# Kernel tuning notes

Measured on AMD Instinct MI355X. Metric: run time of the kernel, lower is better.

Reference implementation:

```python
import jax, jax.numpy as jnp
import numpy as np

DIM = 512
BATCH, SEQ = 4, 4096


def setup_inputs() -> dict:
    key = jax.random.key(0)
    kx, kq, kk, kv, ko = jax.random.split(key, 5)
    s = DIM ** -0.5  # fan-in style init scale for stability
    return {
        "x": jax.random.normal(kx, (BATCH, SEQ, DIM), dtype=jnp.float32),
        "Wq": jax.random.normal(kq, (DIM, DIM), dtype=jnp.float32) * s,
        "Wk": jax.random.normal(kk, (DIM, DIM), dtype=jnp.float32) * s,
        "Wv": jax.random.normal(kv, (DIM, DIM), dtype=jnp.float32) * s,
        "Wo": jax.random.normal(ko, (DIM, DIM), dtype=jnp.float32) * s,
    }


def reference(x, Wq, Wk, Wv, Wo):
    # x: [B, S, D]; projections (torch Linear, no bias -> x @ W here)
    q = jnp.einsum('bsd,dk->bsk', x, Wq)  # [B,S,K]
    k = jnp.einsum('bsd,dk->bsk', x, Wk)  # [B,S,K]
    v = jnp.einsum('bsd,dv->bsv', x, Wv)  # [B,S,V]

    # sequential recurrence: M_t = M_{t-1} + v_t k_t^T ; y_t = M_t q_t
    def step(M, qkv_t):
        q_t, k_t, v_t = qkv_t  # each [B, K] / [B, V]
        M = M + v_t[:, :, None] * k_t[:, None, :]  # [B, V, K]
        y_t = jnp.einsum('bvk,bk->bv', M, q_t)
        return M, y_t

    M0 = jnp.zeros((x.shape[0], Wv.shape[1], Wk.shape[1]), dtype=x.dtype)
    qT = jnp.swapaxes(q, 0, 1)  # [S,B,K]
    kT = jnp.swapaxes(k, 0, 1)
    vT = jnp.swapaxes(v, 0, 1)
    _, ys = jax.lax.scan(step, M0, (qT, kT, vT))  # ys: [S,B,V]
    y = jnp.swapaxes(ys, 0, 1)  # [B,S,V]
    return jnp.einsum('bsv,vd->bsd', y, Wo)
```

## Files before the change

### kernel.cpp

```cpp
#include <hip/hip_runtime.h>
#include <hip/hip_bf16.h>

typedef __attribute__((ext_vector_type(8))) short bf16x8;
typedef __attribute__((ext_vector_type(4))) float f32x4;

__device__ inline short f2bf(float f) {
    __hip_bfloat16 h = __float2bfloat16(f);
    short s;
    __builtin_memcpy(&s, &h, 2);
    return s;
}
__device__ inline float bf2f(short s) {
    unsigned int u = ((unsigned int)(unsigned short)s) << 16;
    float f;
    __builtin_memcpy(&f, &u, 4);
    return f;
}

__device__ inline void cp16_async(const void* g, void* l) {
    __builtin_amdgcn_global_load_lds(
        (const __attribute__((address_space(1))) void*)g,
        (__attribute__((address_space(3))) void*)l, 16, 0, 0);
}

__global__ void prep_kernel(const float* __restrict__ x, short* __restrict__ Xp,
                            const float* __restrict__ W0, const float* __restrict__ W1,
                            const float* __restrict__ W2, const float* __restrict__ W3,
                            short* __restrict__ PW, short* __restrict__ WoT) {
    int bid = blockIdx.x;
    if (bid < 4096) {
        int f = bid * 256 + threadIdx.x;
        int mtf = f >> 13, r = f & 8191, kb = r >> 7, row = r & 127;
        const float* src = x + ((size_t)(mtf * 128 + row) * 512 + kb * 8);
        float4 a = ((const float4*)src)[0];
        float4 bq = ((const float4*)src)[1];
        short t[8];
        t[0] = f2bf(a.x);  t[1] = f2bf(a.y);  t[2] = f2bf(a.z);  t[3] = f2bf(a.w);
        t[4] = f2bf(bq.x); t[5] = f2bf(bq.y); t[6] = f2bf(bq.z); t[7] = f2bf(bq.w);
        ((int4*)Xp)[f] = *(const int4*)t;
    } else if (bid < 4480) {
        int g = (bid - 4096) * 256 + threadIdx.x;
        int lane = g & 63, ksg = (g >> 6) & 15, nn = g >> 10;
        int w = nn >> 5;
        int nl = (nn & 31) * 16 + (lane & 15);
        int k0 = ksg * 32 + (lane >> 4) * 8;
        const float* W = (w == 0) ? W0 : (w == 1) ? W1 : W2;
        short t[8];
#pragma unroll
        for (int e = 0; e < 8; ++e) t[e] = f2bf(W[(size_t)(k0 + e) * 512 + nl]);
        ((int4*)PW)[g] = *(const int4*)t;
    } else {
        int i = (bid - 4480) * 256 + threadIdx.x;
        int n = i >> 9, k = i & 511;
        WoT[i] = f2bf(W3[k * 512 + n]);
    }
}


#define KSTEP(ks) { \
    bf16x8 af[4], bfr[4]; \
    _Pragma("unroll") for (int i = 0; i < 4; ++i) \
        af[i] = *(const bf16x8*)&Xs[((ks) * 512 + quad * 128 + wm * 64 + i * 16 + lr) * 8]; \
    _Pragma("unroll") for (int j = 0; j < 4; ++j) \
        bfr[j] = *(const bf16x8*)&PB[((size_t)((j * 16 + (ks)) * 64 + lane)) * 8]; \
    _Pragma("unroll") for (int i = 0; i < 4; ++i) \
        _Pragma("unroll") for (int j = 0; j < 4; ++j) \
            acc[i * 4 + j] = __builtin_amdgcn_mfma_f32_16x16x32_bf16(af[i], bfr[j], acc[i * 4 + j], 0, 0, 0); }

__global__ __launch_bounds__(512, 2) void proj_qkv(const short* __restrict__ Xp,
                                                   const short* __restrict__ PW,
                                                   short* __restrict__ Qb, short* __restrict__ Kb,
                                                   short* __restrict__ Vt, short* __restrict__ Kt) {
    __shared__ short Xs[65536];
    const int tid = threadIdx.x, lane = tid & 63, wv = tid >> 6;
    const int lr = lane & 15, quad = lane >> 4;
    const int wm = wv >> 2, wn = wv & 3;
    const int bid = blockIdx.x;
    const int swz = (bid & 7) * 32 + (bid >> 3);
    const int mt = swz >> 1, half = swz & 1;
    const short* Ap = Xp + (size_t)mt * 65536;
#pragma unroll
    for (int j = 0; j < 8; ++j) {
        const int f = j * 512 + tid;
        cp16_async(Ap + (size_t)f * 8, (char*)Xs + f * 16);
    }
    __builtin_amdgcn_sched_barrier(0);
#pragma unroll
    for (int j = 8; j < 16; ++j) {
        const int f = j * 512 + tid;
        cp16_async(Ap + (size_t)f * 8, (char*)Xs + f * 16);
    }
    __builtin_amdgcn_sched_barrier(0);
    const int b = mt >> 5;
    const int tl0 = (mt & 31) * 128 + wm * 64;
    const int trow0 = mt * 128 + wm * 64;
    for (int pass = 0; pass < 3; ++pass) {
        const int gc0 = half * 768 + pass * 256;
        f32x4 acc[16];
#pragma unroll
        for (int i = 0; i < 16; ++i) acc[i] = (f32x4){0.f, 0.f, 0.f, 0.f};
        const short* PB = PW + (size_t)((gc0 >> 4) + wn * 4) * 8192;
        if (pass == 0) {
            asm volatile("s_waitcnt vmcnt(8)" ::: "memory");
            __builtin_amdgcn_sched_barrier(0);
            __builtin_amdgcn_s_barrier();
            __builtin_amdgcn_sched_barrier(0);
#pragma unroll 4
            for (int ks = 0; ks < 8; ++ks) KSTEP(ks)
            __builtin_amdgcn_sched_barrier(0);
            asm volatile("s_waitcnt vmcnt(0)" ::: "memory");
            __builtin_amdgcn_sched_barrier(0);
            __builtin_amdgcn_s_barrier();
            __builtin_amdgcn_sched_barrier(0);
#pragma unroll 4
            for (int ks = 8; ks < 16; ++ks) KSTEP(ks)
        } else {
#pragma unroll 4
            for (int ks = 0; ks < 16; ++ks) KSTEP(ks)
        }
        const int p = gc0 >> 9;
        const int fc0 = (gc0 & 511) + wn * 64;
        if (p < 2) {
            short* C = p ? Kb : Qb;
#pragma unroll
            for (int i = 0; i < 4; ++i)
#pragma unroll
                for (int j = 0; j < 4; ++j) {
                    const size_t base = (size_t)(trow0 + i * 16 + quad * 4) * 512 + fc0 + j * 16 + lr;
#pragma unroll
                    for (int r = 0; r < 4; ++r)
                        C[base + (size_t)r * 512] = f2bf(acc[i * 4 + j][r]);
                }
        }
        if (p >= 1) {
            short* T = (p == 1) ? Kt : Vt;
#pragma unroll
            for (int i = 0; i < 4; ++i)
#pragma unroll
                for (int j = 0; j < 4; ++j) {
                    const int f = fc0 + j * 16 + lr;
                    short tmp[4];
#pragma unroll
                    for (int r = 0; r < 4; ++r) tmp[r] = f2bf(acc[i * 4 + j][r]);
                    *(int2*)&T[((size_t)b * 512 + f) * 4096 + tl0 + i * 16 + quad * 4] = *(const int2*)tmp;
                }
        }
    }
}


#define LDS_DECL __shared__ short sm[8][4096]

__device__ inline void stage32(const short* __restrict__ A, int lda,
                               const short* __restrict__ B, int ldb, int k0,
                               short* sA, short* sB, int tid) {
#pragma unroll
    for (int j = 0; j < 2; ++j) {
        const int L = tid * 16 + j * 4096;
        const int row = L >> 6;
        const int cb = (L & 63) ^ ((row & 3) << 4);
        cp16_async((const char*)(A + (size_t)row * lda + k0) + cb, (char*)sA + L);
        cp16_async((const char*)(B + (size_t)row * ldb + k0) + cb, (char*)sB + L);
    }
}

__device__ inline void compute32(const short* sA, const short* sB, f32x4* acc,
                                 int wr, int wc, int lr, int quad) {
    const int cb = (quad * 16) ^ ((lr & 3) << 4);
    bf16x8 af[4], bfr[4];
#pragma unroll
    for (int i = 0; i < 4; ++i)
        af[i] = *(const bf16x8*)((const char*)sA + (wr + i * 16 + lr) * 64 + cb);
#pragma unroll
    for (int j = 0; j < 4; ++j)
        bfr[j] = *(const bf16x8*)((const char*)sB + (wc + j * 16 + lr) * 64 + cb);
#pragma unroll
    for (int i = 0; i < 4; ++i)
#pragma unroll
        for (int j = 0; j < 4; ++j)
            acc[i * 4 + j] = __builtin_amdgcn_mfma_f32_16x16x32_bf16(af[i], bfr[j], acc[i * 4 + j], 0, 0, 0);
}

__device__ inline void kloop_pipe(const short* __restrict__ A, int lda,
                                  const short* __restrict__ B, int ldb, int Kd,
                                  f32x4* acc, short (*sm)[4096]) {
    const int tid = threadIdx.x, lane = tid & 63, wv = tid >> 6;
    const int quad = lane >> 4, lr = lane & 15;
    const int wr = (wv >> 1) * 64, wc = (wv & 1) * 64;
    const int NT = Kd >> 5;
    stage32(A, lda, B, ldb, 0,  sm[0], sm[1], tid);
    stage32(A, lda, B, ldb, 32, sm[2], sm[3], tid);
    stage32(A, lda, B, ldb, 64, sm[4], sm[5], tid);
    __builtin_amdgcn_sched_barrier(0);
    asm volatile("s_waitcnt vmcnt(8)" ::: "memory");
    __builtin_amdgcn_sched_barrier(0);
    __builtin_amdgcn_s_barrier();
    __builtin_amdgcn_sched_barrier(0);
    for (int t = 0; t < NT; ++t) {
        const int cur = (t & 3) << 1;
        if (t + 3 < NT)
            stage32(A, lda, B, ldb, (t + 3) << 5,
                    sm[((t + 3) & 3) << 1], sm[(((t + 3) & 3) << 1) + 1], tid);
        __builtin_amdgcn_sched_barrier(0);
        compute32(sm[cur], sm[cur + 1], acc, wr, wc, lr, quad);
        __builtin_amdgcn_sched_barrier(0);
        if (t + 3 < NT) {
            asm volatile("s_waitcnt vmcnt(8)" ::: "memory");
        } else if (t + 2 < NT) {
            asm volatile("s_waitcnt vmcnt(4)" ::: "memory");
        } else {
            asm volatile("s_waitcnt vmcnt(0)" ::: "memory");
        }
        __builtin_amdgcn_sched_barrier(0);
        __builtin_amdgcn_s_barrier();
        __builtin_amdgcn_sched_barrier(0);
    }
}

__device__ inline void store_out(float* p, float v) { *p = v; }
__device__ inline void store_out(short* p, float v) { *p = f2bf(v); }

template <typename OutT>
__device__ inline void store_tile128(OutT* C, int ldc, const f32x4* acc) {
    const int lane = threadIdx.x & 63, wv = threadIdx.x >> 6;
    const int quad = lane >> 4, lr = lane & 15;
    const int wr = (wv >> 1) * 64, wc = (wv & 1) * 64;
#pragma unroll
    for (int i = 0; i < 4; ++i)
#pragma unroll
        for (int j = 0; j < 4; ++j)
#pragma unroll
            for (int r = 0; r < 4; ++r)
                store_out(&C[(size_t)(wr + i * 16 + quad * 4 + r) * ldc + wc + j * 16 + lr],
                          acc[i * 4 + j][r]);
}


__global__ __launch_bounds__(256, 2) void phaseA(const short* __restrict__ Vt,
                                                 const short* __restrict__ Kt,
                                                 short* __restrict__ AM) {
    LDS_DECL;
    const int bc = blockIdx.z, b = bc >> 4, c = bc & 15;
    const short* Ap = Vt + ((size_t)b * 512 + blockIdx.x * 128) * 4096 + c * 256;
    const short* Bp = Kt + ((size_t)b * 512 + blockIdx.y * 128) * 4096 + c * 256;
    short* Cp = AM + (size_t)bc * 262144 + (size_t)blockIdx.x * 128 * 512 + blockIdx.y * 128;
    f32x4 acc[16];
#pragma unroll
    for (int i = 0; i < 16; ++i) acc[i] = (f32x4){0.f, 0.f, 0.f, 0.f};
    kloop_pipe(Ap, 4096, Bp, 4096, 256, acc, sm);
    store_tile128(Cp, 512, acc);
}

__global__ __launch_bounds__(256, 2) void scan_phaseS(short* __restrict__ AM,
                                                      const short* __restrict__ Q,
                                                      const short* __restrict__ K,
                                                      short* __restrict__ P) {
    LDS_DECL;
    if (blockIdx.x < 512) {
        int i = blockIdx.x * 256 + threadIdx.x;
        int b = i >> 15;
        int vk8 = i & 32767;
        size_t base = (size_t)b * 16 * 262144 + (size_t)vk8 * 8;
        float acc[8];
#pragma unroll
        for (int s = 0; s < 8; ++s) acc[s] = 0.f;
        for (int c = 0; c < 16; ++c) {
            short* p = AM + base + (size_t)c * 262144;
            short in8[8];
            *(int4*)in8 = *(const int4*)p;
            short out8[8];
#pragma unroll
            for (int s = 0; s < 8; ++s) out8[s] = f2bf(acc[s]);
            *(int4*)p = *(const int4*)out8;
#pragma unroll
            for (int s = 0; s < 8; ++s) acc[s] += bf2f(in8[s]);
        }
        return;
    }
    const int e = blockIdx.x - 512;
    const int bc = e >> 2, mt = e & 1, nt = (e >> 1) & 1;
    if (mt < nt) return;
    const int b = bc >> 4, c = bc & 15;
    short* Pt = P + (size_t)bc * 65536 + (size_t)mt * 128 * 256 + nt * 128;
    const short* Ap = Q + ((size_t)(b * 4096 + c * 256 + mt * 128)) * 512;
    const short* Bp = K + ((size_t)(b * 4096 + c * 256 + nt * 128)) * 512;
    f32x4 acc[16];
#pragma unroll
    for (int i = 0; i < 16; ++i) acc[i] = (f32x4){0.f, 0.f, 0.f, 0.f};
    kloop_pipe(Ap, 512, Bp, 512, 512, acc, sm);
    const int lane = threadIdx.x & 63, wv = threadIdx.x >> 6;
    const int quad = lane >> 4, lr = lane & 15;
    const int wr = (wv >> 1) * 64, wc = (wv & 1) * 64;
    const bool diag = (mt == nt);
#pragma unroll
    for (int i = 0; i < 4; ++i)
#pragma unroll
        for (int j = 0; j < 4; ++j)
#pragma unroll
            for (int r = 0; r < 4; ++r) {
                int t = wr + i * 16 + quad * 4 + r;
                int jj = wc + j * 16 + lr;
                float v = (!diag || jj <= t) ? acc[i * 4 + j][r] : 0.f;
                Pt[(size_t)t * 256 + jj] = f2bf(v);
            }
}

__global__ __launch_bounds__(256, 2) void phaseY(const short* __restrict__ Q,
                                                 const short* __restrict__ Mpre,
                                                 const short* __restrict__ P,
                                                 const short* __restrict__ Vt,
                                                 short* __restrict__ Y) {
    LDS_DECL;
    const int bc = blockIdx.z, b = bc >> 4, c = bc & 15;
    const int mt = blockIdx.x, nt = blockIdx.y;
    f32x4 acc[16];
#pragma unroll
    for (int i = 0; i < 16; ++i) acc[i] = (f32x4){0.f, 0.f, 0.f, 0.f};
    const short* Ai = Q + ((size_t)(b * 4096 + c * 256 + mt * 128)) * 512;
    const short* Bi = Mpre + (size_t)bc * 262144 + (size_t)nt * 128 * 512;
    kloop_pipe(Ai, 512, Bi, 512, 512, acc, sm);
    const short* Ap = P + (size_t)bc * 65536 + (size_t)mt * 128 * 256;
    const short* Bv = Vt + ((size_t)b * 512 + nt * 128) * 4096 + c * 256;
    kloop_pipe(Ap, 256, Bv, 4096, (mt + 1) * 128, acc, sm);
    short* Cp = Y + ((size_t)(b * 4096 + c * 256 + mt * 128)) * 512 + nt * 128;
    store_tile128(Cp, 512, acc);
}

template <typename OutT>
__global__ __launch_bounds__(256, 2) void gemm128(const short* __restrict__ A, int lda,
                                                  const short* __restrict__ B, int ldb,
                                                  OutT* __restrict__ C, int ldc, int Kd) {
    LDS_DECL;
    const short* At = A + (size_t)blockIdx.x * 128 * lda;
    const short* Bt = B + (size_t)blockIdx.y * 128 * ldb;
    OutT* Ct = C + (size_t)blockIdx.x * 128 * ldc + blockIdx.y * 128;
    f32x4 acc[16];
#pragma unroll
    for (int i = 0; i < 16; ++i) acc[i] = (f32x4){0.f, 0.f, 0.f, 0.f};
    kloop_pipe(At, lda, Bt, ldb, Kd, acc, sm);
    store_tile128(Ct, ldc, acc);
}


extern "C" void kernel_launch(void* const* d_in, const int* in_sizes, int n_in,
                              void* d_out, int out_size, void* d_ws, size_t ws_size,
                              hipStream_t stream) {
    const float* x  = (const float*)d_in[0];
    const float* Wq = (const float*)d_in[1];
    const float* Wk = (const float*)d_in[2];
    const float* Wv = (const float*)d_in[3];
    const float* Wo = (const float*)d_in[4];
    float* out = (float*)d_out;

    const size_t NTD = 16384 * 512;

    short* ws  = (short*)d_ws;
    short* Xp  = ws;
    short* Qb  = Xp + NTD;
    short* Kb  = Qb + NTD;
    short* Kt  = Kb + NTD;
    short* Vt  = Kt + NTD;
    short* P   = Vt + NTD;
    short* W4T = P + 4194304;
    short* AM  = W4T + 1048576;
    short* Yb  = Kb;

    short* PW  = W4T;
    short* WoT = W4T + 786432;

    prep_kernel<<<5504, 256, 0, stream>>>(x, Xp, Wq, Wk, Wv, Wo, PW, WoT);
    proj_qkv<<<256, 512, 0, stream>>>(Xp, PW, Qb, Kb, Vt, Kt);
    phaseA<<<dim3(4, 4, 64), 256, 0, stream>>>(Vt, Kt, AM);
    scan_phaseS<<<768, 256, 0, stream>>>(AM, Qb, Kb, P);
    phaseY<<<dim3(2, 4, 64), 256, 0, stream>>>(Qb, AM, P, Vt, Yb);
    gemm128<float><<<dim3(128, 4), 256, 0, stream>>>(Yb, 512, WoT, 512, out, 512, 512);
}
```

Baseline: 223.7 us.

## Replace pipelined 128x128 GEMMs with LDS-resident A-panel kernels streaming B from global

Rewrites phaseA, scan_phaseS, phaseY and the output GEMM to use 512-thread blocks. Each block stages one full A panel into swizzled LDS once, and each wave reads its B fragments straight from global memory instead of running a 4-stage double-tile LDS pipeline. Larger per-block tiles reduce the number of blocks and the amount of redundant A traffic. The output GEMM is transposed so each lane writes a float4 vector. The cost is B loads that skip LDS and are not coalesced across waves, fewer blocks to fill the GPU, and more accumulators per thread in phaseA.

```diff
diff --git a/kernel.cpp b/kernel.cpp
--- a/kernel.cpp
+++ b/kernel.cpp
@@ -22,6 +22,7 @@
         (const __attribute__((address_space(1))) void*)g,
         (__attribute__((address_space(3))) void*)l, 16, 0, 0);
 }
+
 
 __global__ void prep_kernel(const float* __restrict__ x, short* __restrict__ Xp,
                             const float* __restrict__ W0, const float* __restrict__ W1,
@@ -71,7 +72,7 @@
                                                    const short* __restrict__ PW,
                                                    short* __restrict__ Qb, short* __restrict__ Kb,
                                                    short* __restrict__ Vt, short* __restrict__ Kt) {
-    __shared__ short Xs[65536];
+    __shared__ __attribute__((aligned(16))) short Xs[65536];
     const int tid = threadIdx.x, lane = tid & 63, wv = tid >> 6;
     const int lr = lane & 15, quad = lane >> 4;
     const int wm = wv >> 2, wn = wv & 3;
@@ -149,115 +150,83 @@
 }
 
 
-#define LDS_DECL __shared__ short sm[8][4096]
-
-__device__ inline void stage32(const short* __restrict__ A, int lda,
-                               const short* __restrict__ B, int ldb, int k0,
-                               short* sA, short* sB, int tid) {
-#pragma unroll
-    for (int j = 0; j < 2; ++j) {
-        const int L = tid * 16 + j * 4096;
-        const int row = L >> 6;
-        const int cb = (L & 63) ^ ((row & 3) << 4);
-        cp16_async((const char*)(A + (size_t)row * lda + k0) + cb, (char*)sA + L);
-        cp16_async((const char*)(B + (size_t)row * ldb + k0) + cb, (char*)sB + L);
-    }
-}
-
-__device__ inline void compute32(const short* sA, const short* sB, f32x4* acc,
-                                 int wr, int wc, int lr, int quad) {
-    const int cb = (quad * 16) ^ ((lr & 3) << 4);
-    bf16x8 af[4], bfr[4];
-#pragma unroll
-    for (int i = 0; i < 4; ++i)
-        af[i] = *(const bf16x8*)((const char*)sA + (wr + i * 16 + lr) * 64 + cb);
-#pragma unroll
-    for (int j = 0; j < 4; ++j)
-        bfr[j] = *(const bf16x8*)((const char*)sB + (wc + j * 16 + lr) * 64 + cb);
-#pragma unroll
-    for (int i = 0; i < 4; ++i)
-#pragma unroll
-        for (int j = 0; j < 4; ++j)
-            acc[i * 4 + j] = __builtin_amdgcn_mfma_f32_16x16x32_bf16(af[i], bfr[j], acc[i * 4 + j], 0, 0, 0);
-}
-
-__device__ inline void kloop_pipe(const short* __restrict__ A, int lda,
-                                  const short* __restrict__ B, int ldb, int Kd,
-                                  f32x4* acc, short (*sm)[4096]) {
-    const int tid = threadIdx.x, lane = tid & 63, wv = tid >> 6;
-    const int quad = lane >> 4, lr = lane & 15;
-    const int wr = (wv >> 1) * 64, wc = (wv & 1) * 64;
-    const int NT = Kd >> 5;
-    stage32(A, lda, B, ldb, 0,  sm[0], sm[1], tid);
-    stage32(A, lda, B, ldb, 32, sm[2], sm[3], tid);
-    stage32(A, lda, B, ldb, 64, sm[4], sm[5], tid);
-    __builtin_amdgcn_sched_barrier(0);
-    asm volatile("s_waitcnt vmcnt(8)" ::: "memory");
-    __builtin_amdgcn_sched_barrier(0);
-    __builtin_amdgcn_s_barrier();
-    __builtin_amdgcn_sched_barrier(0);
-    for (int t = 0; t < NT; ++t) {
-        const int cur = (t & 3) << 1;
-        if (t + 3 < NT)
-            stage32(A, lda, B, ldb, (t + 3) << 5,
-                    sm[((t + 3) & 3) << 1], sm[(((t + 3) & 3) << 1) + 1], tid);
-        __builtin_amdgcn_sched_barrier(0);
-        compute32(sm[cur], sm[cur + 1], acc, wr, wc, lr, quad);
-        __builtin_amdgcn_sched_barrier(0);
-        if (t + 3 < NT) {
-            asm volatile("s_waitcnt vmcnt(8)" ::: "memory");
-        } else if (t + 2 < NT) {
-            asm volatile("s_waitcnt vmcnt(4)" ::: "memory");
-        } else {
-            asm volatile("s_waitcnt vmcnt(0)" ::: "memory");
-        }
-        __builtin_amdgcn_sched_barrier(0);
-        __builtin_amdgcn_s_barrier();
-        __builtin_amdgcn_sched_barrier(0);
-    }
-}
-
-__device__ inline void store_out(float* p, float v) { *p = v; }
-__device__ inline void store_out(short* p, float v) { *p = f2bf(v); }
-
-template <typename OutT>
-__device__ inline void store_tile128(OutT* C, int ldc, const f32x4* acc) {
-    const int lane = threadIdx.x & 63, wv = threadIdx.x >> 6;
-    const int quad = lane >> 4, lr = lane & 15;
-    const int wr = (wv >> 1) * 64, wc = (wv & 1) * 64;
-#pragma unroll
-    for (int i = 0; i < 4; ++i)
-#pragma unroll
-        for (int j = 0; j < 4; ++j)
-#pragma unroll
-            for (int r = 0; r < 4; ++r)
-                store_out(&C[(size_t)(wr + i * 16 + quad * 4 + r) * ldc + wc + j * 16 + lr],
-                          acc[i * 4 + j][r]);
-}
-
-
-__global__ __launch_bounds__(256, 2) void phaseA(const short* __restrict__ Vt,
+template <int SH>
+__device__ inline void stage_panel(const short* __restrict__ G, int lda_s,
+                                   short* lds, int tid) {
+    constexpr int NF = 1 << SH;
+#pragma unroll
+    for (int j = 0; j < NF / 4; ++j) {
+        const int s = j * 512 + tid;
+        const int row = s >> SH;
+        const int X = (s & (NF - 1)) ^ (row & 7);
+        cp16_async(G + (size_t)row * lda_s + X * 8, (char*)lds + s * 16);
+    }
+}
+
+template <int SH, int NJ>
+__device__ inline void kstep_pg(const short* __restrict__ Apan, int ks,
+                                const short* __restrict__ B, int ldb_s, int kb,
+                                int mbase, int lr, int quad, f32x4* acc) {
+    bf16x8 af[4], bfr[NJ];
+#pragma unroll
+    for (int i = 0; i < 4; ++i) {
+        const int mr = mbase + i * 16 + lr;
+        af[i] = *(const bf16x8*)&Apan[((mr << SH) + ((ks * 4 + quad) ^ (mr & 7))) * 8];
+    }
+#pragma unroll
+    for (int j = 0; j < NJ; ++j)
+        bfr[j] = *(const bf16x8*)&B[(size_t)(j * 16 + lr) * ldb_s + kb + quad * 8];
+#pragma unroll
+    for (int i = 0; i < 4; ++i)
+#pragma unroll
+        for (int j = 0; j < NJ; ++j)
+            acc[i * NJ + j] = __builtin_amdgcn_mfma_f32_16x16x32_bf16(af[i], bfr[j], acc[i * NJ + j], 0, 0, 0);
+}
+
+#define WAIT_BAR(N) \
+    __builtin_amdgcn_sched_barrier(0); \
+    asm volatile("s_waitcnt vmcnt(" #N ")" ::: "memory"); \
+    __builtin_amdgcn_sched_barrier(0); \
+    __builtin_amdgcn_s_barrier(); \
+    __builtin_amdgcn_sched_barrier(0);
+
+__global__ __launch_bounds__(512, 2) void phaseA(const short* __restrict__ Vt,
                                                  const short* __restrict__ Kt,
                                                  short* __restrict__ AM) {
-    LDS_DECL;
-    const int bc = blockIdx.z, b = bc >> 4, c = bc & 15;
-    const short* Ap = Vt + ((size_t)b * 512 + blockIdx.x * 128) * 4096 + c * 256;
-    const short* Bp = Kt + ((size_t)b * 512 + blockIdx.y * 128) * 4096 + c * 256;
-    short* Cp = AM + (size_t)bc * 262144 + (size_t)blockIdx.x * 128 * 512 + blockIdx.y * 128;
-    f32x4 acc[16];
-#pragma unroll
-    for (int i = 0; i < 16; ++i) acc[i] = (f32x4){0.f, 0.f, 0.f, 0.f};
-    kloop_pipe(Ap, 4096, Bp, 4096, 256, acc, sm);
-    store_tile128(Cp, 512, acc);
-}
-
-__global__ __launch_bounds__(256, 2) void scan_phaseS(short* __restrict__ AM,
+    __shared__ __attribute__((aligned(16))) short Apan[32768];
+    const int tid = threadIdx.x, lane = tid & 63, wv = tid >> 6;
+    const int lr = lane & 15, quad = lane >> 4;
+    const int wm = wv >> 2, wn = wv & 3;
+    const int ft = blockIdx.x, bc = blockIdx.z, b = bc >> 4, c = bc & 15;
+    stage_panel<5>(Vt + ((size_t)(b * 512 + ft * 128)) * 4096 + c * 256, 4096, Apan, tid);
+    WAIT_BAR(0)
+    const short* Bk = Kt + ((size_t)(b * 512 + wn * 128)) * 4096 + c * 256;
+    f32x4 acc[32];
+#pragma unroll
+    for (int i = 0; i < 32; ++i) acc[i] = (f32x4){0.f, 0.f, 0.f, 0.f};
+#pragma unroll 4
+    for (int ks = 0; ks < 8; ++ks)
+        kstep_pg<5, 8>(Apan, ks, Bk, 4096, ks * 32, wm * 64, lr, quad, acc);
+    short* Cp = AM + (size_t)bc * 262144;
+#pragma unroll
+    for (int i = 0; i < 4; ++i)
+#pragma unroll
+        for (int j = 0; j < 8; ++j) {
+            const int v = ft * 128 + wm * 64 + i * 16 + quad * 4;
+            const int k = wn * 128 + j * 16 + lr;
+#pragma unroll
+            for (int r = 0; r < 4; ++r)
+                Cp[(size_t)(v + r) * 512 + k] = f2bf(acc[i * 8 + j][r]);
+        }
+}
+
+__global__ __launch_bounds__(512, 2) void scan_phaseS(short* __restrict__ AM,
                                                       const short* __restrict__ Q,
                                                       const short* __restrict__ K,
                                                       short* __restrict__ P) {
-    LDS_DECL;
-    if (blockIdx.x < 512) {
-        int i = blockIdx.x * 256 + threadIdx.x;
+    __shared__ __attribute__((aligned(16))) short Qpan[65536];
+    if (blockIdx.x < 256) {
+        int i = blockIdx.x * 512 + threadIdx.x;
         int b = i >> 15;
         int vk8 = i & 32767;
         size_t base = (size_t)b * 16 * 262144 + (size_t)vk8 * 8;
@@ -277,68 +246,109 @@
         }
         return;
     }
-    const int e = blockIdx.x - 512;
-    const int bc = e >> 2, mt = e & 1, nt = (e >> 1) & 1;
-    if (mt < nt) return;
-    const int b = bc >> 4, c = bc & 15;
-    short* Pt = P + (size_t)bc * 65536 + (size_t)mt * 128 * 256 + nt * 128;
-    const short* Ap = Q + ((size_t)(b * 4096 + c * 256 + mt * 128)) * 512;
-    const short* Bp = K + ((size_t)(b * 4096 + c * 256 + nt * 128)) * 512;
+    const int e = blockIdx.x - 256;
+    const int bc = e >> 1, mt = e & 1, b = bc >> 4, c = bc & 15;
+    const int tid = threadIdx.x, lane = tid & 63, wv = tid >> 6;
+    const int lr = lane & 15, quad = lane >> 4;
+    const int wm = wv >> 2, wn = wv & 3;
+    stage_panel<6>(Q + (size_t)(b * 4096 + c * 256 + mt * 128) * 512, 512, Qpan, tid);
+    WAIT_BAR(0)
+    const short* Bk = K + (size_t)(b * 4096 + c * 256 + wn * 64) * 512;
     f32x4 acc[16];
 #pragma unroll
     for (int i = 0; i < 16; ++i) acc[i] = (f32x4){0.f, 0.f, 0.f, 0.f};
-    kloop_pipe(Ap, 512, Bp, 512, 512, acc, sm);
-    const int lane = threadIdx.x & 63, wv = threadIdx.x >> 6;
-    const int quad = lane >> 4, lr = lane & 15;
-    const int wr = (wv >> 1) * 64, wc = (wv & 1) * 64;
-    const bool diag = (mt == nt);
+#pragma unroll 4
+    for (int ks = 0; ks < 16; ++ks)
+        kstep_pg<6, 4>(Qpan, ks, Bk, 512, ks * 32, wm * 64, lr, quad, acc);
+    if (mt == 0 && wn >= 2) return;
+    short* Pt = P + (size_t)bc * 65536;
 #pragma unroll
     for (int i = 0; i < 4; ++i)
 #pragma unroll
         for (int j = 0; j < 4; ++j)
 #pragma unroll
             for (int r = 0; r < 4; ++r) {
-                int t = wr + i * 16 + quad * 4 + r;
-                int jj = wc + j * 16 + lr;
-                float v = (!diag || jj <= t) ? acc[i * 4 + j][r] : 0.f;
-                Pt[(size_t)t * 256 + jj] = f2bf(v);
+                const int trow = mt * 128 + wm * 64 + i * 16 + quad * 4 + r;
+                const int jcol = wn * 64 + j * 16 + lr;
+                Pt[(size_t)trow * 256 + jcol] = f2bf(jcol <= trow ? acc[i * 4 + j][r] : 0.f);
             }
 }
 
-__global__ __launch_bounds__(256, 2) void phaseY(const short* __restrict__ Q,
+__global__ __launch_bounds__(512, 2) void phaseY(const short* __restrict__ Q,
                                                  const short* __restrict__ Mpre,
                                                  const short* __restrict__ P,
                                                  const short* __restrict__ Vt,
                                                  short* __restrict__ Y) {
-    LDS_DECL;
-    const int bc = blockIdx.z, b = bc >> 4, c = bc & 15;
-    const int mt = blockIdx.x, nt = blockIdx.y;
+    __shared__ __attribute__((aligned(16))) short Ppan[32768];
+    __shared__ __attribute__((aligned(16))) short Qpan[32768];
+    const int tid = threadIdx.x, lane = tid & 63, wv = tid >> 6;
+    const int lr = lane & 15, quad = lane >> 4;
+    const int wm = wv >> 2, wn = wv & 3;
+    const int mt = blockIdx.x, nh = blockIdx.y, bc = blockIdx.z, b = bc >> 4, c = bc & 15;
+    const short* Qrow = Q + (size_t)(b * 4096 + c * 256 + mt * 128) * 512;
+    stage_panel<5>(P + (size_t)bc * 65536 + mt * 32768, 256, Ppan, tid);
+    __builtin_amdgcn_sched_barrier(0);
+    stage_panel<5>(Qrow, 512, Qpan, tid);
+    WAIT_BAR(8)
     f32x4 acc[16];
 #pragma unroll
     for (int i = 0; i < 16; ++i) acc[i] = (f32x4){0.f, 0.f, 0.f, 0.f};
-    const short* Ai = Q + ((size_t)(b * 4096 + c * 256 + mt * 128)) * 512;
-    const short* Bi = Mpre + (size_t)bc * 262144 + (size_t)nt * 128 * 512;
-    kloop_pipe(Ai, 512, Bi, 512, 512, acc, sm);
-    const short* Ap = P + (size_t)bc * 65536 + (size_t)mt * 128 * 256;
-    const short* Bv = Vt + ((size_t)b * 512 + nt * 128) * 4096 + c * 256;
-    kloop_pipe(Ap, 256, Bv, 4096, (mt + 1) * 128, acc, sm);
-    short* Cp = Y + ((size_t)(b * 4096 + c * 256 + mt * 128)) * 512 + nt * 128;
-    store_tile128(Cp, 512, acc);
-}
-
-template <typename OutT>
-__global__ __launch_bounds__(256, 2) void gemm128(const short* __restrict__ A, int lda,
-                                                  const short* __restrict__ B, int ldb,
-                                                  OutT* __restrict__ C, int ldc, int Kd) {
-    LDS_DECL;
-    const short* At = A + (size_t)blockIdx.x * 128 * lda;
-    const short* Bt = B + (size_t)blockIdx.y * 128 * ldb;
-    OutT* Ct = C + (size_t)blockIdx.x * 128 * ldc + blockIdx.y * 128;
+    const short* Bv = Vt + (size_t)(b * 512 + nh * 256 + wn * 64) * 4096 + c * 256;
+#pragma unroll
+    for (int ks = 0; ks < 4; ++ks)
+        kstep_pg<5, 4>(Ppan, ks, Bv, 4096, ks * 32, wm * 64, lr, quad, acc);
+    if (mt) {
+#pragma unroll
+        for (int ks = 4; ks < 8; ++ks)
+            kstep_pg<5, 4>(Ppan, ks, Bv, 4096, ks * 32, wm * 64, lr, quad, acc);
+    }
+    WAIT_BAR(0)
+    stage_panel<5>(Qrow + 256, 512, Ppan, tid);
+    __builtin_amdgcn_sched_barrier(0);
+    const short* Bm = Mpre + (size_t)bc * 262144 + (size_t)(nh * 256 + wn * 64) * 512;
+#pragma unroll 4
+    for (int ks = 0; ks < 8; ++ks)
+        kstep_pg<5, 4>(Qpan, ks, Bm, 512, ks * 32, wm * 64, lr, quad, acc);
+    WAIT_BAR(0)
+#pragma unroll 4
+    for (int ks = 0; ks < 8; ++ks)
+        kstep_pg<5, 4>(Ppan, ks, Bm, 512, 256 + ks * 32, wm * 64, lr, quad, acc);
+    short* Yt = Y + (size_t)(b * 4096 + c * 256 + mt * 128) * 512 + nh * 256;
+#pragma unroll
+    for (int i = 0; i < 4; ++i)
+#pragma unroll
+        for (int j = 0; j < 4; ++j)
+#pragma unroll
+            for (int r = 0; r < 4; ++r)
+                Yt[(size_t)(wm * 64 + i * 16 + quad * 4 + r) * 512 + wn * 64 + j * 16 + lr] =
+                    f2bf(acc[i * 4 + j][r]);
+}
+
+__global__ __launch_bounds__(512, 2) void gemm_out(const short* __restrict__ Yb,
+                                                   const short* __restrict__ WoT,
+                                                   float* __restrict__ out) {
+    __shared__ __attribute__((aligned(16))) short Wpan[65536];
+    const int tid = threadIdx.x, lane = tid & 63, wv = tid >> 6;
+    const int lr = lane & 15, quad = lane >> 4;
+    const int wm = wv >> 2, wn = wv & 3;
+    const int dt = blockIdx.x, tc = blockIdx.y;
+    stage_panel<6>(WoT + (size_t)dt * 65536, 512, Wpan, tid);
+    WAIT_BAR(0)
+    const short* By = Yb + (size_t)(tc * 256 + wn * 64) * 512;
     f32x4 acc[16];
 #pragma unroll
     for (int i = 0; i < 16; ++i) acc[i] = (f32x4){0.f, 0.f, 0.f, 0.f};
-    kloop_pipe(At, lda, Bt, ldb, Kd, acc, sm);
-    store_tile128(Ct, ldc, acc);
+#pragma unroll 4
+    for (int ks = 0; ks < 16; ++ks)
+        kstep_pg<6, 4>(Wpan, ks, By, 512, ks * 32, wm * 64, lr, quad, acc);
+#pragma unroll
+    for (int i = 0; i < 4; ++i)
+#pragma unroll
+        for (int j = 0; j < 4; ++j) {
+            const int d0 = dt * 128 + wm * 64 + i * 16 + quad * 4;
+            const int t = tc * 256 + wn * 64 + j * 16 + lr;
+            *(f32x4*)&out[(size_t)t * 512 + d0] = acc[i * 4 + j];
+        }
 }
 
 
@@ -370,8 +380,8 @@
 
     prep_kernel<<<5504, 256, 0, stream>>>(x, Xp, Wq, Wk, Wv, Wo, PW, WoT);
     proj_qkv<<<256, 512, 0, stream>>>(Xp, PW, Qb, Kb, Vt, Kt);
-    phaseA<<<dim3(4, 4, 64), 256, 0, stream>>>(Vt, Kt, AM);
-    scan_phaseS<<<768, 256, 0, stream>>>(AM, Qb, Kb, P);
-    phaseY<<<dim3(2, 4, 64), 256, 0, stream>>>(Qb, AM, P, Vt, Yb);
-    gemm128<float><<<dim3(128, 4), 256, 0, stream>>>(Yb, 512, WoT, 512, out, 512, 512);
-}
+    phaseA<<<dim3(4, 1, 64), 512, 0, stream>>>(Vt, Kt, AM);
+    scan_phaseS<<<384, 512, 0, stream>>>(AM, Qb, Kb, P);
+    phaseY<<<dim3(2, 2, 64), 512, 0, stream>>>(Qb, AM, P, Vt, Yb);
+    gemm_out<<<dim3(4, 64), 512, 0, stream>>>(Yb, WoT, out);
+}
```

New measurement: 241.8 us. 8.1% more time.

## Pre-pack K and Y into MFMA fragment layout and rework phaseA/out GEMMs

Applied to the files above, without the earlier changes.

proj_qkv now writes K transposed directly in a packed MFMA B-fragment layout, and phaseY writes Y in a similar packed layout. phaseA and the output GEMM are rewritten as 512-thread kernels that stage only the A panel in swizzled LDS once and stream the pre-packed B operand straight from global memory into registers, replacing the generic pipelined LDS k-loop. The output GEMM computes the transposed product so it can store float4 vectors. The aim is to cut LDS staging and barrier overhead and get more coalesced operand loads. The cost is tightly coupled layout index math across kernels and B fragments that are no longer shared through LDS.

```diff
diff --git a/kernel.cpp b/kernel.cpp
--- a/kernel.cpp
+++ b/kernel.cpp
@@ -22,6 +22,7 @@
         (const __attribute__((address_space(1))) void*)g,
         (__attribute__((address_space(3))) void*)l, 16, 0, 0);
 }
+
 
 __global__ void prep_kernel(const float* __restrict__ x, short* __restrict__ Xp,
                             const float* __restrict__ W0, const float* __restrict__ W1,
@@ -70,8 +71,8 @@
 __global__ __launch_bounds__(512, 2) void proj_qkv(const short* __restrict__ Xp,
                                                    const short* __restrict__ PW,
                                                    short* __restrict__ Qb, short* __restrict__ Kb,
-                                                   short* __restrict__ Vt, short* __restrict__ Kt) {
-    __shared__ short Xs[65536];
+                                                   short* __restrict__ Vt, short* __restrict__ PKt) {
+    __shared__ __attribute__((aligned(16))) short Xs[65536];
     const int tid = threadIdx.x, lane = tid & 63, wv = tid >> 6;
     const int lr = lane & 15, quad = lane >> 4;
     const int wm = wv >> 2, wn = wv & 3;
@@ -132,20 +133,107 @@
                         C[base + (size_t)r * 512] = f2bf(acc[i * 4 + j][r]);
                 }
         }
-        if (p >= 1) {
-            short* T = (p == 1) ? Kt : Vt;
-#pragma unroll
-            for (int i = 0; i < 4; ++i)
+        if (p == 1) {
+#pragma unroll
+            for (int i = 0; i < 4; ++i) {
+                const int T0 = tl0 + i * 16 + quad * 4;
+                const int c = T0 >> 8, tin = T0 & 255;
+                const int ts = tin >> 5, tq = (tin & 31) >> 3, e0 = T0 & 7;
 #pragma unroll
                 for (int j = 0; j < 4; ++j) {
                     const int f = fc0 + j * 16 + lr;
                     short tmp[4];
 #pragma unroll
                     for (int r = 0; r < 4; ++r) tmp[r] = f2bf(acc[i * 4 + j][r]);
-                    *(int2*)&T[((size_t)b * 512 + f) * 4096 + tl0 + i * 16 + quad * 4] = *(const int2*)tmp;
+                    const size_t a = (size_t)(b * 16 + c) * 131072 +
+                                     (size_t)(((f >> 4) * 8 + ts) * 64 + tq * 16 + (f & 15)) * 8 + e0;
+                    *(int2*)&PKt[a] = *(const int2*)tmp;
                 }
-        }
-    }
+            }
+        } else if (p == 2) {
+#pragma unroll
+            for (int i = 0; i < 4; ++i)
+#pragma unroll
+                for (int j = 0; j < 4; ++j) {
+                    const int f = fc0 + j * 16 + lr;
+                    short tmp[4];
+#pragma unroll
+                    for (int r = 0; r < 4; ++r) tmp[r] = f2bf(acc[i * 4 + j][r]);
+                    *(int2*)&Vt[((size_t)b * 512 + f) * 4096 + tl0 + i * 16 + quad * 4] = *(const int2*)tmp;
+                }
+        }
+    }
+}
+
+
+template <int SH>
+__device__ inline void stage_panel(const short* __restrict__ G, int lda_s,
+                                   short* lds, int tid) {
+    constexpr int NF = 1 << SH;
+#pragma unroll
+    for (int j = 0; j < NF / 4; ++j) {
+        const int s = j * 512 + tid;
+        const int row = s >> SH;
+        const int X = (s & (NF - 1)) ^ (row & 7);
+        cp16_async(G + (size_t)row * lda_s + X * 8, (char*)lds + s * 16);
+    }
+}
+
+template <int SH, int NJ, int NS>
+__device__ inline void kstep_pb(const short* __restrict__ Apan, int ks,
+                                const short* __restrict__ PB, int lane,
+                                int mbase, int lr, int quad, f32x4* acc) {
+    bf16x8 af[4], bfr[NJ];
+#pragma unroll
+    for (int i = 0; i < 4; ++i) {
+        const int mr = mbase + i * 16 + lr;
+        af[i] = *(const bf16x8*)&Apan[((mr << SH) + ((ks * 4 + quad) ^ (mr & 7))) * 8];
+    }
+#pragma unroll
+    for (int j = 0; j < NJ; ++j)
+        bfr[j] = *(const bf16x8*)&PB[((size_t)((j * NS + ks) * 64 + lane)) * 8];
+#pragma unroll
+    for (int i = 0; i < 4; ++i)
+#pragma unroll
+        for (int j = 0; j < NJ; ++j)
+            acc[i * NJ + j] = __builtin_amdgcn_mfma_f32_16x16x32_bf16(af[i], bfr[j], acc[i * NJ + j], 0, 0, 0);
+}
+
+#define WAIT_BAR(N) \
+    __builtin_amdgcn_sched_barrier(0); \
+    asm volatile("s_waitcnt vmcnt(" #N ")" ::: "memory"); \
+    __builtin_amdgcn_sched_barrier(0); \
+    __builtin_amdgcn_s_barrier(); \
+    __builtin_amdgcn_sched_barrier(0);
+
+__global__ __launch_bounds__(512, 2) void phaseA(const short* __restrict__ Vt,
+                                                 const short* __restrict__ PKt,
+                                                 short* __restrict__ AM) {
+    __shared__ __attribute__((aligned(16))) short Apan[32768];
+    const int tid = threadIdx.x, lane = tid & 63, wv = tid >> 6;
+    const int lr = lane & 15, quad = lane >> 4;
+    const int wm = wv >> 2, wn = wv & 3;
+    const int ft = blockIdx.x, kh = blockIdx.y, bc = blockIdx.z, b = bc >> 4, c = bc & 15;
+    stage_panel<5>(Vt + ((size_t)(b * 512 + ft * 128)) * 4096 + c * 256, 4096, Apan, tid);
+    WAIT_BAR(0)
+    const short* PB = PKt + (size_t)bc * 131072 + (size_t)(kh * 16 + wn * 4) * 4096;
+    f32x4 acc[16];
+#pragma unroll
+    for (int i = 0; i < 16; ++i) acc[i] = (f32x4){0.f, 0.f, 0.f, 0.f};
+#pragma unroll
+    for (int ks = 0; ks < 8; ++ks)
+        kstep_pb<5, 4, 8>(Apan, ks, PB, lane, wm * 64, lr, quad, acc);
+    short* Cp = AM + (size_t)bc * 262144;
+#pragma unroll
+    for (int i = 0; i < 4; ++i)
+#pragma unroll
+        for (int j = 0; j < 4; ++j) {
+            const int v = ft * 128 + wm * 64 + i * 16 + quad * 4;
+            const int k = kh * 256 + wn * 64 + j * 16 + lr;
+#pragma unroll
+            for (int r = 0; r < 4; ++r)
+                Cp[(size_t)(v + r) * 512 + k] = f2bf(acc[i * 4 + j][r]);
+        }
 }
 
 
@@ -217,40 +305,6 @@
     }
 }
 
-__device__ inline void store_out(float* p, float v) { *p = v; }
-__device__ inline void store_out(short* p, float v) { *p = f2bf(v); }
-
-template <typename OutT>
-__device__ inline void store_tile128(OutT* C, int ldc, const f32x4* acc) {
-    const int lane = threadIdx.x & 63, wv = threadIdx.x >> 6;
-    const int quad = lane >> 4, lr = lane & 15;
-    const int wr = (wv >> 1) * 64, wc = (wv & 1) * 64;
-#pragma unroll
-    for (int i = 0; i < 4; ++i)
-#pragma unroll
-        for (int j = 0; j < 4; ++j)
-#pragma unroll
-            for (int r = 0; r < 4; ++r)
-                store_out(&C[(size_t)(wr + i * 16 + quad * 4 + r) * ldc + wc + j * 16 + lr],
-                          acc[i * 4 + j][r]);
-}
-
-
-__global__ __launch_bounds__(256, 2) void phaseA(const short* __restrict__ Vt,
-                                                 const short* __restrict__ Kt,
-                                                 short* __restrict__ AM) {
-    LDS_DECL;
-    const int bc = blockIdx.z, b = bc >> 4, c = bc & 15;
-    const short* Ap = Vt + ((size_t)b * 512 + blockIdx.x * 128) * 4096 + c * 256;
-    const short* Bp = Kt + ((size_t)b * 512 + blockIdx.y * 128) * 4096 + c * 256;
-    short* Cp = AM + (size_t)bc * 262144 + (size_t)blockIdx.x * 128 * 512 + blockIdx.y * 128;
-    f32x4 acc[16];
-#pragma unroll
-    for (int i = 0; i < 16; ++i) acc[i] = (f32x4){0.f, 0.f, 0.f, 0.f};
-    kloop_pipe(Ap, 4096, Bp, 4096, 256, acc, sm);
-    store_tile128(Cp, 512, acc);
-}
-
 __global__ __launch_bounds__(256, 2) void scan_phaseS(short* __restrict__ AM,
                                                       const short* __restrict__ Q,
                                                       const short* __restrict__ K,
@@ -309,7 +363,7 @@
                                                  const short* __restrict__ Mpre,
                                                  const short* __restrict__ P,
                                                  const short* __restrict__ Vt,
-                                                 short* __restrict__ Y) {
+                                                 short* __restrict__ PYb) {
     LDS_DECL;
     const int bc = blockIdx.z, b = bc >> 4, c = bc & 15;
     const int mt = blockIdx.x, nt = blockIdx.y;
@@ -322,23 +376,49 @@
     const short* Ap = P + (size_t)bc * 65536 + (size_t)mt * 128 * 256;
     const short* Bv = Vt + ((size_t)b * 512 + nt * 128) * 4096 + c * 256;
     kloop_pipe(Ap, 256, Bv, 4096, (mt + 1) * 128, acc, sm);
-    short* Cp = Y + ((size_t)(b * 4096 + c * 256 + mt * 128)) * 512 + nt * 128;
-    store_tile128(Cp, 512, acc);
-}
-
-template <typename OutT>
-__global__ __launch_bounds__(256, 2) void gemm128(const short* __restrict__ A, int lda,
-                                                  const short* __restrict__ B, int ldb,
-                                                  OutT* __restrict__ C, int ldc, int Kd) {
-    LDS_DECL;
-    const short* At = A + (size_t)blockIdx.x * 128 * lda;
-    const short* Bt = B + (size_t)blockIdx.y * 128 * ldb;
-    OutT* Ct = C + (size_t)blockIdx.x * 128 * ldc + blockIdx.y * 128;
+    const int lane = threadIdx.x & 63, wv = threadIdx.x >> 6;
+    const int quad = lane >> 4, lr = lane & 15;
+    const int wr = (wv >> 1) * 64, wc = (wv & 1) * 64;
+    const int Tbase = b * 4096 + c * 256 + mt * 128 + wr;
+#pragma unroll
+    for (int i = 0; i < 4; ++i) {
+        const int tg = (Tbase + i * 16) >> 4;
+#pragma unroll
+        for (int j = 0; j < 4; ++j) {
+            const int v = nt * 128 + wc + j * 16 + lr;
+            const size_t base = ((size_t)(tg * 16 + (v >> 5)) * 64 + ((v & 31) >> 3) * 16 + quad * 4) * 8 + (v & 7);
+#pragma unroll
+            for (int r = 0; r < 4; ++r)
+                PYb[base + (size_t)r * 8] = f2bf(acc[i * 4 + j][r]);
+        }
+    }
+}
+
+__global__ __launch_bounds__(512, 2) void gemm_out(const short* __restrict__ PYb,
+                                                   const short* __restrict__ WoT,
+                                                   float* __restrict__ out) {
+    __shared__ __attribute__((aligned(16))) short Wpan[65536];
+    const int tid = threadIdx.x, lane = tid & 63, wv = tid >> 6;
+    const int lr = lane & 15, quad = lane >> 4;
+    const int wm = wv >> 2, wn = wv & 3;
+    const int dt = blockIdx.x, tc = blockIdx.y;
+    stage_panel<6>(WoT + (size_t)dt * 65536, 512, Wpan, tid);
+    WAIT_BAR(0)
+    const short* PB = PYb + (size_t)(tc * 16 + wn * 4) * 8192;
     f32x4 acc[16];
 #pragma unroll
     for (int i = 0; i < 16; ++i) acc[i] = (f32x4){0.f, 0.f, 0.f, 0.f};
-    kloop_pipe(At, lda, Bt, ldb, Kd, acc, sm);
-    store_tile128(Ct, ldc, acc);
+#pragma unroll 4
+    for (int ks = 0; ks < 16; ++ks)
+        kstep_pb<6, 4, 16>(Wpan, ks, PB, lane, wm * 64, lr, quad, acc);
+#pragma unroll
+    for (int i = 0; i < 4; ++i)
+#pragma unroll
+        for (int j = 0; j < 4; ++j) {
+            const int d0 = dt * 128 + wm * 64 + i * 16 + quad * 4;
+            const int t = tc * 256 + wn * 64 + j * 16 + lr;
+            *(f32x4*)&out[(size_t)t * 512 + d0] = acc[i * 4 + j];
+        }
 }
 
 
@@ -358,20 +438,20 @@
     short* Xp  = ws;
     short* Qb  = Xp + NTD;
     short* Kb  = Qb + NTD;
-    short* Kt  = Kb + NTD;
-    short* Vt  = Kt + NTD;
+    short* PKt = Kb + NTD;
+    short* Vt  = PKt + NTD;
     short* P   = Vt + NTD;
     short* W4T = P + 4194304;
     short* AM  = W4T + 1048576;
-    short* Yb  = Kb;
+    short* PYb = Kb;
 
     short* PW  = W4T;
     short* WoT = W4T + 786432;
 
     prep_kernel<<<5504, 256, 0, stream>>>(x, Xp, Wq, Wk, Wv, Wo, PW, WoT);
-    proj_qkv<<<256, 512, 0, stream>>>(Xp, PW, Qb, Kb, Vt, Kt);
-    phaseA<<<dim3(4, 4, 64), 256, 0, stream>>>(Vt, Kt, AM);
+    proj_qkv<<<256, 512, 0, stream>>>(Xp, PW, Qb, Kb, Vt, PKt);
+    phaseA<<<dim3(4, 2, 64), 512, 0, stream>>>(Vt, PKt, AM);
     scan_phaseS<<<768, 256, 0, stream>>>(AM, Qb, Kb, P);
-    phaseY<<<dim3(2, 4, 64), 256, 0, stream>>>(Qb, AM, P, Vt, Yb);
-    gemm128<float><<<dim3(128, 4), 256, 0, stream>>>(Yb, 512, WoT, 512, out, 512, 512);
-}
+    phaseY<<<dim3(2, 4, 64), 256, 0, stream>>>(Qb, AM, P, Vt, PYb);
+    gemm_out<<<dim3(4, 64), 512, 0, stream>>>(PYb, WoT, out);
+}
```

Result: slower. 229.9 us (+2.8%).
